# Kernel tuning notes

Measured on AMD Instinct MI355X. Metric: run time of the kernel, lower is better.

## Reference

```python
import jax, jax.numpy as jnp
import numpy as np
from jax import lax

WINDOW = 8
MAX_VAL = 1.0
C1 = (0.01 * MAX_VAL) ** 2
C2 = (0.03 * MAX_VAL) ** 2


def _box_sum(x):
    # Equivalent to conv2d with an all-ones WINDOW x WINDOW kernel, groups=C, VALID padding.
    return lax.reduce_window(x, 0.0, lax.add,
                             window_dimensions=(1, 1, WINDOW, WINDOW),
                             window_strides=(1, 1, 1, 1),
                             padding='VALID')


def setup_inputs() -> dict:
    key = jax.random.key(0)
    k1, k2 = jax.random.split(key)
    shape = (32, 3, 512, 512)  # NCHW, C=3 per groups=3 conv
    groundtruth = jax.random.uniform(k1, shape, dtype=jnp.float32)
    noisy_img = jax.random.uniform(k2, shape, dtype=jnp.float32)
    return {"groundtruth": groundtruth, "noisy_img": noisy_img}


def reference(groundtruth, noisy_img):
    mu1 = _box_sum(groundtruth)
    mu2 = _box_sum(noisy_img)
    mu1_sq = mu1 * mu1
    mu2_sq = mu2 * mu2
    mu1_mu2 = mu1 * mu2
    sigma1_sq = _box_sum(groundtruth * groundtruth) - mu1_sq
    sigma2_sq = _box_sum(noisy_img * noisy_img) - mu2_sq
    sigma12 = _box_sum(groundtruth * noisy_img) - mu1_mu2
    ssim_map = ((2.0 * mu1_mu2 + C1) * (2.0 * sigma12 + C2)) / (
        (mu1_sq + mu2_sq + C1) * (sigma1_sq + sigma2_sq + C2))
    return jnp.mean(1.0 - ssim_map)
```

## Files before the change

kernel.cpp:

```cpp
#include <hip/hip_runtime.h>


#define W 512
#define H 512
#define OW 505
#define OH 505
#define TH 16
#define NSTRIP ((OH + TH - 1) / TH)
#define NIMG 96
#define NPIX (96.0 * 505.0 * 505.0)

__device__ __forceinline__ float4 ld4(const float* p) { return *(const float4*)p; }
__device__ __forceinline__ float4 f4add(float4 a, float4 b) {
    return make_float4(a.x + b.x, a.y + b.y, a.z + b.z, a.w + b.w);
}
__device__ __forceinline__ float4 f4sub(float4 a, float4 b) {
    return make_float4(a.x - b.x, a.y - b.y, a.z - b.z, a.w - b.w);
}
__device__ __forceinline__ float4 f4mul(float4 a, float4 b) {
    return make_float4(a.x * b.x, a.y * b.y, a.z * b.z, a.w * b.w);
}

__global__ void finalize(const double* p, float* out) {
    out[0] = 1.0f - (float)(*p / NPIX);
}

__global__ void __launch_bounds__(64, 2)
ssim_main(const float* __restrict__ gt, const float* __restrict__ ni,
          double* __restrict__ acc_out)
{
    const int lane = threadIdx.x;
    const int img  = blockIdx.y;
    const int R0   = blockIdx.x * TH;
    const int R1   = min(R0 + TH, OH);
    const int c0   = lane * 8;

    const float C1 = 1e-4f, C2 = 9e-4f;

    const float* gx = gt + (size_t)img * (W * H) + c0;
    const float* gy = ni + (size_t)img * (W * H) + c0;

    __shared__ float vbuf[4][520];

    float4 rx[8][2], ry[8][2];

    float4 vsx0 = make_float4(0,0,0,0), vsx1 = make_float4(0,0,0,0);
    float4 vsy0 = make_float4(0,0,0,0), vsy1 = make_float4(0,0,0,0);
    float4 vsq0 = make_float4(0,0,0,0), vsq1 = make_float4(0,0,0,0);
    float4 vsp0 = make_float4(0,0,0,0), vsp1 = make_float4(0,0,0,0);

#pragma unroll
    for (int k = 0; k < 7; ++k) {
        const float* bx = gx + (size_t)(R0 + k) * W;
        const float* by = gy + (size_t)(R0 + k) * W;
        float4 x0 = ld4(bx), x1 = ld4(bx + 4);
        float4 y0 = ld4(by), y1 = ld4(by + 4);
        rx[k][0] = x0; rx[k][1] = x1; ry[k][0] = y0; ry[k][1] = y1;
        vsx0 = f4add(vsx0, x0); vsx1 = f4add(vsx1, x1);
        vsy0 = f4add(vsy0, y0); vsy1 = f4add(vsy1, y1);
        vsq0 = f4add(vsq0, f4add(f4mul(x0,x0), f4mul(y0,y0)));
        vsq1 = f4add(vsq1, f4add(f4mul(x1,x1), f4mul(y1,y1)));
        vsp0 = f4add(vsp0, f4mul(x0,y0));
        vsp1 = f4add(vsp1, f4mul(x1,y1));
    }
    rx[7][0] = rx[7][1] = ry[7][0] = ry[7][1] = make_float4(0,0,0,0);

    float4 pfx[2][2], pfy[2][2];
    {
        const float* bx = gx + (size_t)(R0 + 7) * W;
        const float* by = gy + (size_t)(R0 + 7) * W;
        pfx[0][0] = ld4(bx); pfx[0][1] = ld4(bx + 4);
        pfy[0][0] = ld4(by); pfy[0][1] = ld4(by + 4);
    }
    {
        const float* bx = gx + (size_t)(R0 + 8) * W;
        const float* by = gy + (size_t)(R0 + 8) * W;
        pfx[1][0] = ld4(bx); pfx[1][1] = ld4(bx + 4);
        pfy[1][0] = ld4(by); pfy[1][1] = ld4(by + 4);
    }

    float acc = 0.0f;

#define HORIZ(S, v, n) {                                                  \
        float T = ((v[0]+v[1])+(v[2]+v[3])) + ((v[4]+v[5])+(v[6]+v[7]));  \
        S[0] = T;                                                         \
        _Pragma("unroll") for (int j = 1; j < 8; ++j)                     \
            S[j] = S[j-1] - v[j-1] + n[j-1];                              \
    }

#define ROWBODY(k, slot) {                                                \
        const int r = rbase + (k);                                        \
        if (r < R1) {                                   \
            const int p = (k) & 1;                                        \
            float4 cx0 = pfx[p][0], cx1 = pfx[p][1];                      \
            float4 cy0 = pfy[p][0], cy1 = pfy[p][1];                      \
            if (r + 2 < R1) {    \
                const float* bx = gx + (size_t)(r + 9) * W;               \
                const float* by = gy + (size_t)(r + 9) * W;               \
                pfx[p][0] = ld4(bx); pfx[p][1] = ld4(bx + 4);             \
                pfy[p][0] = ld4(by); pfy[p][1] = ld4(by + 4);             \
            }                                                             \
            float4 ox0 = rx[slot][0], ox1 = rx[slot][1];                  \
            float4 oy0 = ry[slot][0], oy1 = ry[slot][1];                  \
            vsx0 = f4add(f4sub(vsx0, ox0), cx0);                          \
            vsx1 = f4add(f4sub(vsx1, ox1), cx1);                          \
            vsy0 = f4add(f4sub(vsy0, oy0), cy0);                          \
            vsy1 = f4add(f4sub(vsy1, oy1), cy1);                          \
            vsq0 = f4add(vsq0, f4sub(f4add(f4mul(cx0,cx0), f4mul(cy0,cy0)), \
                                     f4add(f4mul(ox0,ox0), f4mul(oy0,oy0)))); \
            vsq1 = f4add(vsq1, f4sub(f4add(f4mul(cx1,cx1), f4mul(cy1,cy1)), \
                                     f4add(f4mul(ox1,ox1), f4mul(oy1,oy1)))); \
            vsp0 = f4add(vsp0, f4sub(f4mul(cx0,cy0), f4mul(ox0,oy0)));    \
            vsp1 = f4add(vsp1, f4sub(f4mul(cx1,cy1), f4mul(ox1,oy1)));    \
            rx[slot][0] = cx0; rx[slot][1] = cx1;                         \
            ry[slot][0] = cy0; ry[slot][1] = cy1;                         \
                                  \
            *(float4*)&vbuf[0][c0] = vsx0; *(float4*)&vbuf[0][c0+4] = vsx1; \
            *(float4*)&vbuf[1][c0] = vsy0; *(float4*)&vbuf[1][c0+4] = vsy1; \
            *(float4*)&vbuf[2][c0] = vsq0; *(float4*)&vbuf[2][c0+4] = vsq1; \
            *(float4*)&vbuf[3][c0] = vsp0; *(float4*)&vbuf[3][c0+4] = vsp1; \
            __builtin_amdgcn_sched_barrier(0);                            \
            __builtin_amdgcn_wave_barrier();                              \
            __builtin_amdgcn_sched_barrier(0);                            \
                       \
            float4 nx0 = *(float4*)&vbuf[0][c0+8], nx1 = *(float4*)&vbuf[0][c0+12]; \
            float4 ny0 = *(float4*)&vbuf[1][c0+8], ny1 = *(float4*)&vbuf[1][c0+12]; \
            float4 nq0 = *(float4*)&vbuf[2][c0+8], nq1 = *(float4*)&vbuf[2][c0+12]; \
            float4 np0 = *(float4*)&vbuf[3][c0+8], np1 = *(float4*)&vbuf[3][c0+12]; \
            float vx[8] = {vsx0.x,vsx0.y,vsx0.z,vsx0.w,vsx1.x,vsx1.y,vsx1.z,vsx1.w}; \
            float vy[8] = {vsy0.x,vsy0.y,vsy0.z,vsy0.w,vsy1.x,vsy1.y,vsy1.z,vsy1.w}; \
            float vq[8] = {vsq0.x,vsq0.y,vsq0.z,vsq0.w,vsq1.x,vsq1.y,vsq1.z,vsq1.w}; \
            float vp[8] = {vsp0.x,vsp0.y,vsp0.z,vsp0.w,vsp1.x,vsp1.y,vsp1.z,vsp1.w}; \
            float nx[8] = {nx0.x,nx0.y,nx0.z,nx0.w,nx1.x,nx1.y,nx1.z,nx1.w}; \
            float ny[8] = {ny0.x,ny0.y,ny0.z,ny0.w,ny1.x,ny1.y,ny1.z,ny1.w}; \
            float nq[8] = {nq0.x,nq0.y,nq0.z,nq0.w,nq1.x,nq1.y,nq1.z,nq1.w}; \
            float np[8] = {np0.x,np0.y,np0.z,np0.w,np1.x,np1.y,np1.z,np1.w}; \
            float Sx[8], Sy[8], Sq[8], Sp[8];                             \
            HORIZ(Sx, vx, nx) HORIZ(Sy, vy, ny)                           \
            HORIZ(Sq, vq, nq) HORIZ(Sp, vp, np)                           \
            _Pragma("unroll")                                             \
            for (int j = 0; j < 8; ++j) {                                 \
                float sx = Sx[j], sy = Sy[j];                             \
                float mu12 = sx * sy;                                     \
                float n1v = 2.0f * mu12 + C1;                             \
                float n2v = 2.0f * (Sp[j] - mu12) + C2;                   \
                float sx2 = sx * sx, sy2 = sy * sy;                       \
                float d1  = sx2 + sy2 + C1;                               \
                float d2  = (Sq[j] - sx2 - sy2) + C2;                     \
                float sv  = (n1v * n2v) * __builtin_amdgcn_rcpf(d1 * d2); \
                if (c0 + j < OW) acc += sv;     \
            }                                                             \
        }                                                                 \
    }

    for (int rbase = R0; rbase < R1; rbase += 8) {
        ROWBODY(0, 7)
        ROWBODY(1, 0)
        ROWBODY(2, 1)
        ROWBODY(3, 2)
        ROWBODY(4, 3)
        ROWBODY(5, 4)
        ROWBODY(6, 5)
        ROWBODY(7, 6)
    }

#pragma unroll
    for (int off = 32; off; off >>= 1) acc += __shfl_down(acc, off);
    if (lane == 0) atomicAdd(acc_out, (double)acc);
}

extern "C" void kernel_launch(void* const* d_in, const int* in_sizes, int n_in,
                              void* d_out, int out_size, void* d_ws, size_t ws_size,
                              hipStream_t stream) {
    const float* gt = (const float*)d_in[0];
    const float* ni = (const float*)d_in[1];
    double* acc = (double*)d_ws;

    hipMemsetAsync(acc, 0, sizeof(double), stream);
    dim3 grid(NSTRIP, NIMG);
    ssim_main<<<grid, 64, 0, stream>>>(gt, ni, acc);
    finalize<<<1, 1, 0, stream>>>(acc, (float*)d_out);
}
```

Measured before the change: 256.4 us.

## Split lane columns into two coalesced float4 halves with double-buffered LDS

```diff
diff --git a/kernel.cpp b/kernel.cpp
--- a/kernel.cpp
+++ b/kernel.cpp
@@ -2,7 +2,6 @@
 
 
 #define W 512
-#define H 512
 #define OW 505
 #define OH 505
 #define TH 16
@@ -21,134 +20,149 @@
     return make_float4(a.x * b.x, a.y * b.y, a.z * b.z, a.w * b.w);
 }
 
+#define FENCE do { __builtin_amdgcn_sched_barrier(0);                      \
+                   __builtin_amdgcn_wave_barrier();                        \
+                   __builtin_amdgcn_sched_barrier(0); } while (0)
+
 __global__ void finalize(const double* p, float* out) {
     out[0] = 1.0f - (float)(*p / NPIX);
 }
 
-__global__ void __launch_bounds__(64, 2)
+__global__ void __launch_bounds__(64, 1)
 ssim_main(const float* __restrict__ gt, const float* __restrict__ ni,
           double* __restrict__ acc_out)
 {
     const int lane = threadIdx.x;
+    const int cA   = lane * 4;
+    const int cB   = 256 + cA;
     const int img  = blockIdx.y;
     const int R0   = blockIdx.x * TH;
     const int R1   = min(R0 + TH, OH);
-    const int c0   = lane * 8;
 
     const float C1 = 1e-4f, C2 = 9e-4f;
 
-    const float* gx = gt + (size_t)img * (W * H) + c0;
-    const float* gy = ni + (size_t)img * (W * H) + c0;
+    const float* gx = gt + (size_t)img * (W * W);
+    const float* gy = ni + (size_t)img * (W * W);
 
-    __shared__ float vbuf[4][520];
+    __shared__ float vbuf[2][4][520];
 
-    float4 rx[8][2], ry[8][2];
+    float4 rxA[8], rxB[8], ryA[8], ryB[8];
 
-    float4 vsx0 = make_float4(0,0,0,0), vsx1 = make_float4(0,0,0,0);
-    float4 vsy0 = make_float4(0,0,0,0), vsy1 = make_float4(0,0,0,0);
-    float4 vsq0 = make_float4(0,0,0,0), vsq1 = make_float4(0,0,0,0);
-    float4 vsp0 = make_float4(0,0,0,0), vsp1 = make_float4(0,0,0,0);
+    float4 vsxA = make_float4(0,0,0,0), vsxB = make_float4(0,0,0,0);
+    float4 vsyA = make_float4(0,0,0,0), vsyB = make_float4(0,0,0,0);
+    float4 vsqA = make_float4(0,0,0,0), vsqB = make_float4(0,0,0,0);
+    float4 vspA = make_float4(0,0,0,0), vspB = make_float4(0,0,0,0);
 
 #pragma unroll
     for (int k = 0; k < 7; ++k) {
         const float* bx = gx + (size_t)(R0 + k) * W;
         const float* by = gy + (size_t)(R0 + k) * W;
-        float4 x0 = ld4(bx), x1 = ld4(bx + 4);
-        float4 y0 = ld4(by), y1 = ld4(by + 4);
-        rx[k][0] = x0; rx[k][1] = x1; ry[k][0] = y0; ry[k][1] = y1;
-        vsx0 = f4add(vsx0, x0); vsx1 = f4add(vsx1, x1);
-        vsy0 = f4add(vsy0, y0); vsy1 = f4add(vsy1, y1);
-        vsq0 = f4add(vsq0, f4add(f4mul(x0,x0), f4mul(y0,y0)));
-        vsq1 = f4add(vsq1, f4add(f4mul(x1,x1), f4mul(y1,y1)));
-        vsp0 = f4add(vsp0, f4mul(x0,y0));
-        vsp1 = f4add(vsp1, f4mul(x1,y1));
+        float4 xA = ld4(bx + cA), xB = ld4(bx + cB);
+        float4 yA = ld4(by + cA), yB = ld4(by + cB);
+        rxA[k] = xA; rxB[k] = xB; ryA[k] = yA; ryB[k] = yB;
+        vsxA = f4add(vsxA, xA); vsxB = f4add(vsxB, xB);
+        vsyA = f4add(vsyA, yA); vsyB = f4add(vsyB, yB);
+        vsqA = f4add(vsqA, f4add(f4mul(xA,xA), f4mul(yA,yA)));
+        vsqB = f4add(vsqB, f4add(f4mul(xB,xB), f4mul(yB,yB)));
+        vspA = f4add(vspA, f4mul(xA,yA));
+        vspB = f4add(vspB, f4mul(xB,yB));
     }
-    rx[7][0] = rx[7][1] = ry[7][0] = ry[7][1] = make_float4(0,0,0,0);
+    rxA[7] = rxB[7] = ryA[7] = ryB[7] = make_float4(0,0,0,0);
 
-    float4 pfx[2][2], pfy[2][2];
+    float4 pfxA[2], pfxB[2], pfyA[2], pfyB[2];
     {
         const float* bx = gx + (size_t)(R0 + 7) * W;
         const float* by = gy + (size_t)(R0 + 7) * W;
-        pfx[0][0] = ld4(bx); pfx[0][1] = ld4(bx + 4);
-        pfy[0][0] = ld4(by); pfy[0][1] = ld4(by + 4);
+        pfxA[0] = ld4(bx + cA); pfxB[0] = ld4(bx + cB);
+        pfyA[0] = ld4(by + cA); pfyB[0] = ld4(by + cB);
     }
     {
         const float* bx = gx + (size_t)(R0 + 8) * W;
         const float* by = gy + (size_t)(R0 + 8) * W;
-        pfx[1][0] = ld4(bx); pfx[1][1] = ld4(bx + 4);
-        pfy[1][0] = ld4(by); pfy[1][1] = ld4(by + 4);
+        pfxA[1] = ld4(bx + cA); pfxB[1] = ld4(bx + cB);
+        pfyA[1] = ld4(by + cA); pfyB[1] = ld4(by + cB);
     }
 
     float acc = 0.0f;
 
-#define HORIZ(S, v, n) {                                                  \
-        float T = ((v[0]+v[1])+(v[2]+v[3])) + ((v[4]+v[5])+(v[6]+v[7]));  \
-        S[0] = T;                                                         \
-        _Pragma("unroll") for (int j = 1; j < 8; ++j)                     \
-            S[j] = S[j-1] - v[j-1] + n[j-1];                              \
+#define HORIZ(q, v, base, Bq) {                                           \
+        float4 n1 = *(float4*)&vbuf[b][q][(base) + 4];                    \
+        float4 n2 = *(float4*)&vbuf[b][q][(base) + 8];                    \
+        float s = ((v.x + v.y) + (v.z + v.w)) +                           \
+                  ((n1.x + n1.y) + (n1.z + n1.w));                        \
+        Bq[0] = s;                                                        \
+        s += n2.x - v.x; Bq[1] = s;                                       \
+        s += n2.y - v.y; Bq[2] = s;                                       \
+        s += n2.z - v.z; Bq[3] = s;                                       \
+    }
+
+#define SSIM4(Bm, colbase, CHECK) {                                       \
+        _Pragma("unroll")                                                 \
+        for (int j = 0; j < 4; ++j) {                                     \
+            float Sx = Bm[0][j], Sy = Bm[1][j];                           \
+            float Sq = Bm[2][j], Sp = Bm[3][j];                           \
+            float mu12 = Sx * Sy;                                         \
+            float n1v = 2.0f * mu12 + C1;                                 \
+            float n2v = 2.0f * (Sp - mu12) + C2;                          \
+            float sx2 = Sx * Sx, sy2 = Sy * Sy;                           \
+            float d1  = sx2 + sy2 + C1;                                   \
+            float d2  = (Sq - sx2 - sy2) + C2;                            \
+            float sv  = (n1v * n2v) * __builtin_amdgcn_rcpf(d1 * d2);     \
+            if (!(CHECK) || ((colbase) + j < OW)) acc += sv;              \
+        }                                                                 \
     }
 
 #define ROWBODY(k, slot) {                                                \
         const int r = rbase + (k);                                        \
         if (r < R1) {                                   \
-            const int p = (k) & 1;                                        \
-            float4 cx0 = pfx[p][0], cx1 = pfx[p][1];                      \
-            float4 cy0 = pfy[p][0], cy1 = pfy[p][1];                      \
-            if (r + 2 < R1) {    \
+            const int b = (k) & 1;                                        \
+            float4 cxA = pfxA[b], cxB = pfxB[b];     \
+            float4 cyA = pfyA[b], cyB = pfyB[b];                          \
+            if (r + 2 < R1) {   \
                 const float* bx = gx + (size_t)(r + 9) * W;               \
                 const float* by = gy + (size_t)(r + 9) * W;               \
-                pfx[p][0] = ld4(bx); pfx[p][1] = ld4(bx + 4);             \
-                pfy[p][0] = ld4(by); pfy[p][1] = ld4(by + 4);             \
+                pfxA[b] = ld4(bx + cA); pfxB[b] = ld4(bx + cB);           \
+                pfyA[b] = ld4(by + cA); pfyB[b] = ld4(by + cB);           \
             }                                                             \
-            float4 ox0 = rx[slot][0], ox1 = rx[slot][1];                  \
-            float4 oy0 = ry[slot][0], oy1 = ry[slot][1];                  \
-            vsx0 = f4add(f4sub(vsx0, ox0), cx0);                          \
-            vsx1 = f4add(f4sub(vsx1, ox1), cx1);                          \
-            vsy0 = f4add(f4sub(vsy0, oy0), cy0);                          \
-            vsy1 = f4add(f4sub(vsy1, oy1), cy1);                          \
-            vsq0 = f4add(vsq0, f4sub(f4add(f4mul(cx0,cx0), f4mul(cy0,cy0)), \
-                                     f4add(f4mul(ox0,ox0), f4mul(oy0,oy0)))); \
-            vsq1 = f4add(vsq1, f4sub(f4add(f4mul(cx1,cx1), f4mul(cy1,cy1)), \
-                                     f4add(f4mul(ox1,ox1), f4mul(oy1,oy1)))); \
-            vsp0 = f4add(vsp0, f4sub(f4mul(cx0,cy0), f4mul(ox0,oy0)));    \
-            vsp1 = f4add(vsp1, f4sub(f4mul(cx1,cy1), f4mul(ox1,oy1)));    \
-            rx[slot][0] = cx0; rx[slot][1] = cx1;                         \
-            ry[slot][0] = cy0; ry[slot][1] = cy1;                         \
-                                  \
-            *(float4*)&vbuf[0][c0] = vsx0; *(float4*)&vbuf[0][c0+4] = vsx1; \
-            *(float4*)&vbuf[1][c0] = vsy0; *(float4*)&vbuf[1][c0+4] = vsy1; \
-            *(float4*)&vbuf[2][c0] = vsq0; *(float4*)&vbuf[2][c0+4] = vsq1; \
-            *(float4*)&vbuf[3][c0] = vsp0; *(float4*)&vbuf[3][c0+4] = vsp1; \
-            __builtin_amdgcn_sched_barrier(0);                            \
-            __builtin_amdgcn_wave_barrier();                              \
-            __builtin_amdgcn_sched_barrier(0);                            \
-                       \
-            float4 nx0 = *(float4*)&vbuf[0][c0+8], nx1 = *(float4*)&vbuf[0][c0+12]; \
-            float4 ny0 = *(float4*)&vbuf[1][c0+8], ny1 = *(float4*)&vbuf[1][c0+12]; \
-            float4 nq0 = *(float4*)&vbuf[2][c0+8], nq1 = *(float4*)&vbuf[2][c0+12]; \
-            float4 np0 = *(float4*)&vbuf[3][c0+8], np1 = *(float4*)&vbuf[3][c0+12]; \
-            float vx[8] = {vsx0.x,vsx0.y,vsx0.z,vsx0.w,vsx1.x,vsx1.y,vsx1.z,vsx1.w}; \
-            float vy[8] = {vsy0.x,vsy0.y,vsy0.z,vsy0.w,vsy1.x,vsy1.y,vsy1.z,vsy1.w}; \
-            float vq[8] = {vsq0.x,vsq0.y,vsq0.z,vsq0.w,vsq1.x,vsq1.y,vsq1.z,vsq1.w}; \
-            float vp[8] = {vsp0.x,vsp0.y,vsp0.z,vsp0.w,vsp1.x,vsp1.y,vsp1.z,vsp1.w}; \
-            float nx[8] = {nx0.x,nx0.y,nx0.z,nx0.w,nx1.x,nx1.y,nx1.z,nx1.w}; \
-            float ny[8] = {ny0.x,ny0.y,ny0.z,ny0.w,ny1.x,ny1.y,ny1.z,ny1.w}; \
-            float nq[8] = {nq0.x,nq0.y,nq0.z,nq0.w,nq1.x,nq1.y,nq1.z,nq1.w}; \
-            float np[8] = {np0.x,np0.y,np0.z,np0.w,np1.x,np1.y,np1.z,np1.w}; \
-            float Sx[8], Sy[8], Sq[8], Sp[8];                             \
-            HORIZ(Sx, vx, nx) HORIZ(Sy, vy, ny)                           \
-            HORIZ(Sq, vq, nq) HORIZ(Sp, vp, np)                           \
-            _Pragma("unroll")                                             \
-            for (int j = 0; j < 8; ++j) {                                 \
-                float sx = Sx[j], sy = Sy[j];                             \
-                float mu12 = sx * sy;                                     \
-                float n1v = 2.0f * mu12 + C1;                             \
-                float n2v = 2.0f * (Sp[j] - mu12) + C2;                   \
-                float sx2 = sx * sx, sy2 = sy * sy;                       \
-                float d1  = sx2 + sy2 + C1;                               \
-                float d2  = (Sq[j] - sx2 - sy2) + C2;                     \
-                float sv  = (n1v * n2v) * __builtin_amdgcn_rcpf(d1 * d2); \
-                if (c0 + j < OW) acc += sv;     \
+            {                              \
+                float4 ox = rxA[slot], oy = ryA[slot];                    \
+                vsxA = f4add(f4sub(vsxA, ox), cxA);                       \
+                vsyA = f4add(f4sub(vsyA, oy), cyA);                       \
+                vsqA = f4add(vsqA, f4sub(f4add(f4mul(cxA,cxA), f4mul(cyA,cyA)), \
+                                         f4add(f4mul(ox,ox),   f4mul(oy,oy)))); \
+                vspA = f4add(vspA, f4sub(f4mul(cxA,cyA), f4mul(ox,oy)));  \
+                rxA[slot] = cxA; ryA[slot] = cyA;                         \
+            }                                                             \
+            {                              \
+                float4 ox = rxB[slot], oy = ryB[slot];                    \
+                vsxB = f4add(f4sub(vsxB, ox), cxB);                       \
+                vsyB = f4add(f4sub(vsyB, oy), cyB);                       \
+                vsqB = f4add(vsqB, f4sub(f4add(f4mul(cxB,cxB), f4mul(cyB,cyB)), \
+                                         f4add(f4mul(ox,ox),   f4mul(oy,oy)))); \
+                vspB = f4add(vspB, f4sub(f4mul(cxB,cyB), f4mul(ox,oy)));  \
+                rxB[slot] = cxB; ryB[slot] = cyB;                         \
+            }                                                             \
+            FENCE;      \
+            *(float4*)&vbuf[b][0][cA] = vsxA;                             \
+            *(float4*)&vbuf[b][0][cB] = vsxB;                             \
+            *(float4*)&vbuf[b][1][cA] = vsyA;                             \
+            *(float4*)&vbuf[b][1][cB] = vsyB;                             \
+            *(float4*)&vbuf[b][2][cA] = vsqA;                             \
+            *(float4*)&vbuf[b][2][cB] = vsqB;                             \
+            *(float4*)&vbuf[b][3][cA] = vspA;                             \
+            *(float4*)&vbuf[b][3][cB] = vspB;                             \
+            FENCE;   \
+            {     \
+                float B4[4][4];                                           \
+                HORIZ(0, vsxA, cA, B4[0]) HORIZ(1, vsyA, cA, B4[1])       \
+                HORIZ(2, vsqA, cA, B4[2]) HORIZ(3, vspA, cA, B4[3])       \
+                SSIM4(B4, cA, 0)                                          \
+            }                                                             \
+            {        \
+                float B4[4][4];                                           \
+                HORIZ(0, vsxB, cB, B4[0]) HORIZ(1, vsyB, cB, B4[1])       \
+                HORIZ(2, vsqB, cB, B4[2]) HORIZ(3, vspB, cB, B4[3])       \
+                SSIM4(B4, cB, 1)                                          \
             }                                                             \
         }                                                                 \
     }
```

Measured after the change: 237.5 us. -7.4%, faster.
